# Performance work log

Hardware: AMD Instinct MI355X
Metric: run time of the kernel (lower is better)

Reference implementation:

```python
import jax, jax.numpy as jnp
import numpy as np

B, S, D, O, E = 8, 4096, 1024, 1024, 64

def setup_inputs() -> dict:
    key = jax.random.key(0)
    kx, kgw, kgb, kew, keb = jax.random.split(key, 5)
    x = jax.random.normal(kx, (B, S, D), dtype=jnp.float32)
    gate_w = jax.random.normal(kgw, (E, D), dtype=jnp.float32) * 0.02
    gate_b = jnp.zeros((E,), dtype=jnp.float32)
    expert_w = jax.random.normal(kew, (E, D, O), dtype=jnp.float32) * 0.02
    expert_b = jnp.zeros((E, O), dtype=jnp.float32)
    return {"x": x, "gate_w": gate_w, "gate_b": gate_b,
            "expert_w": expert_w, "expert_b": expert_b}

def reference(x, gate_w, gate_b, expert_w, expert_b):
    # x: [B,S,D] -> flatten tokens. With world_size=1 the all-reduce and
    # all-to-alls in the torch module are identities, and per-chunk processing
    # is token-independent, so one global pass is mathematically identical.
    b, s, d = x.shape
    xt = x.reshape(-1, d)                                   # [N, D]
    logits = xt @ gate_w.T + gate_b                         # [N, E]
    gates = jax.nn.softmax(logits, axis=-1)
    sel = jnp.argmax(gates, axis=-1)                        # [N] top-1 expert
    order = jnp.argsort(sel)                                # stable sort by expert
    xs = xt[order]                                          # tokens grouped by expert
    counts = jnp.bincount(sel, length=E).astype(jnp.int32)  # tokens per expert
    # Grouped expert GEMM: row block e of xs multiplies expert_w[e].
    ys = jax.lax.ragged_dot(xs, expert_w, counts)           # [N, O]
    ys = ys + expert_b[sel[order]]
    # Combine: scatter sorted outputs back to original token positions.
    # (Note: torch output is NOT scaled by gate probability.)
    out = jnp.zeros((xt.shape[0], expert_w.shape[-1]), dtype=ys.dtype)
    out = out.at[order].set(ys)
    return out.reshape(b, s, -1)
```

## Files before the change

### kernel.cpp

```cpp
#include <hip/hip_runtime.h>
#include <hip/hip_bf16.h>

#define N_TOK 32768
#define DIM 1024
#define OUTD 1024
#define NEXP 64

typedef __attribute__((ext_vector_type(4))) float f32x4;
typedef __attribute__((ext_vector_type(8))) short bf16x8;

__device__ __forceinline__ unsigned short f2bf(float f) {
    unsigned int u = __builtin_bit_cast(unsigned int, f);
    u += 0x7FFFu + ((u >> 16) & 1u);
    return (unsigned short)(u >> 16);
}

#define GLOAD16(gp, lp) \
    __builtin_amdgcn_global_load_lds((const __attribute__((address_space(1))) void*)(gp), \
                                     (__attribute__((address_space(3))) void*)(lp), 16, 0, 0)

__global__ __launch_bounds__(256) void prep_kernel(const float* __restrict__ x,
        const float* __restrict__ gw, const float* __restrict__ gb,
        const float* __restrict__ ew,
        int* __restrict__ sel, int* __restrict__ nflag, int* __restrict__ flags,
        int* __restrict__ counts,
        unsigned short* __restrict__ xb, unsigned short* __restrict__ wt)
{
    __shared__ __align__(16) char smem[18688];
    int tid = threadIdx.x;

    if (blockIdx.x < 512) {
        float (*xs)[36]  = (float(*)[36])smem;
        float (*wsm)[36] = (float(*)[36])(smem + 9216);
        int* h = (int*)(smem + 18432);
        if (tid < NEXP) h[tid] = 0;
        int t0 = blockIdx.x * 64;
        int tg = tid >> 4, eg = tid & 15;

        float acc[4][4];
#pragma unroll
        for (int i = 0; i < 4; i++)
#pragma unroll
            for (int j = 0; j < 4; j++) acc[i][j] = 0.f;

        for (int k0 = 0; k0 < DIM; k0 += 32) {
            __syncthreads();
#pragma unroll
            for (int q = 0; q < 2; q++) {
                int cidx = tid + q * 256;
                int r = cidx >> 3, c4 = (cidx & 7) * 4;
                *reinterpret_cast<float4*>(&xs[r][c4]) =
                    *reinterpret_cast<const float4*>(&x[(size_t)(t0 + r) * DIM + k0 + c4]);
                *reinterpret_cast<float4*>(&wsm[r][c4]) =
                    *reinterpret_cast<const float4*>(&gw[(size_t)r * DIM + k0 + c4]);
            }
            __syncthreads();
            if (xb) {
                int r = tid >> 2, cc = (tid & 3) * 8;
                float4 v0 = *reinterpret_cast<const float4*>(&xs[r][cc]);
                float4 v1 = *reinterpret_cast<const float4*>(&xs[r][cc + 4]);
                uint4 p;
                p.x = (unsigned int)f2bf(v0.x) | ((unsigned int)f2bf(v0.y) << 16);
                p.y = (unsigned int)f2bf(v0.z) | ((unsigned int)f2bf(v0.w) << 16);
                p.z = (unsigned int)f2bf(v1.x) | ((unsigned int)f2bf(v1.y) << 16);
                p.w = (unsigned int)f2bf(v1.z) | ((unsigned int)f2bf(v1.w) << 16);
                *reinterpret_cast<uint4*>(&xb[(size_t)(t0 + r) * DIM + k0 + cc]) = p;
            }
#pragma unroll
            for (int kk4 = 0; kk4 < 8; kk4++) {
                float4 xv[4], wv[4];
#pragma unroll
                for (int i = 0; i < 4; i++)
                    xv[i] = *reinterpret_cast<const float4*>(&xs[tg + 16 * i][kk4 * 4]);
#pragma unroll
                for (int j = 0; j < 4; j++)
                    wv[j] = *reinterpret_cast<const float4*>(&wsm[eg + 16 * j][kk4 * 4]);
#pragma unroll
                for (int i = 0; i < 4; i++)
#pragma unroll
                    for (int j = 0; j < 4; j++) {
                        acc[i][j] = fmaf(xv[i].x, wv[j].x, acc[i][j]);
                        acc[i][j] = fmaf(xv[i].y, wv[j].y, acc[i][j]);
                        acc[i][j] = fmaf(xv[i].z, wv[j].z, acc[i][j]);
                        acc[i][j] = fmaf(xv[i].w, wv[j].w, acc[i][j]);
                    }
            }
        }
#pragma unroll
        for (int j = 0; j < 4; j++) {
            float b = gb[eg + 16 * j];
#pragma unroll
            for (int i = 0; i < 4; i++) acc[i][j] += b;
        }
#pragma unroll
        for (int i = 0; i < 4; i++) {
            float m1 = -1e30f, m2 = -1e30f; int e1 = 0;
#pragma unroll
            for (int j = 0; j < 4; j++) {
                float v = acc[i][j]; int e = eg + 16 * j;
                if (v > m1) { m2 = m1; m1 = v; e1 = e; }
                else if (v > m2) m2 = v;
            }
#pragma unroll
            for (int d = 1; d < 16; d <<= 1) {
                float om1 = __shfl_xor(m1, d, 16);
                float om2 = __shfl_xor(m2, d, 16);
                int   oe1 = __shfl_xor(e1, d, 16);
                if (om1 > m1 || (om1 == m1 && oe1 < e1)) {
                    m2 = fmaxf(om2, m1); m1 = om1; e1 = oe1;
                } else {
                    m2 = fmaxf(m2, om1);
                }
            }
            if (eg == 0) {
                int t = t0 + tg + 16 * i;
                sel[t] = e1;
                atomicAdd(&h[e1], 1);
                if (m1 - m2 < 1e-3f) {
                    int idx = atomicAdd(nflag, 1);
                    if (idx < 4096) flags[idx] = t;
                }
            }
        }
        __syncthreads();
        if (tid < NEXP && h[tid]) atomicAdd(&counts[tid], h[tid]);
    } else {
        if (!wt) return;
        unsigned short* ts = (unsigned short*)smem;
        int lin = blockIdx.x - 512;
        int e = lin >> 8;
        int d0 = (lin & 15) * 64, o0 = ((lin >> 4) & 15) * 64;
        const float* src = ew + (size_t)e * (DIM * OUTD);
        int og = tid & 7;
        int dl = tid >> 3;
#pragma unroll
        for (int i = 0; i < 2; i++) {
            int d = dl + 32 * i;
            const float* sr = &src[(size_t)(d0 + d) * OUTD + o0 + og * 8];
            float4 v0 = *reinterpret_cast<const float4*>(sr);
            float4 v1 = *reinterpret_cast<const float4*>(sr + 4);
            unsigned short b[8] = { f2bf(v0.x), f2bf(v0.y), f2bf(v0.z), f2bf(v0.w),
                                    f2bf(v1.x), f2bf(v1.y), f2bf(v1.z), f2bf(v1.w) };
            int dg = d >> 3, dr = d & 7;
#pragma unroll
            for (int k = 0; k < 8; k++) {
                int o = og * 8 + k;
                int key = (o & 7) ^ ((o >> 3) & 7);
                ts[o * 72 + ((dg ^ key) << 3) + dr] = b[k];
            }
        }
        __syncthreads();
        unsigned short* dst = wt + (size_t)e * (DIM * OUTD);
        int dc = tid & 7;
        int ol = tid >> 3;
#pragma unroll
        for (int i = 0; i < 2; i++) {
            int o = ol + 32 * i;
            int key = (o & 7) ^ ((o >> 3) & 7);
            uint4 v = *reinterpret_cast<const uint4*>(&ts[o * 72 + ((dc ^ key) << 3)]);
            *reinterpret_cast<uint4*>(&dst[(size_t)(o0 + o) * DIM + d0 + dc * 8]) = v;
        }
    }
}

__global__ __launch_bounds__(64) void gate_fix_kernel(const float* __restrict__ x,
        const float* __restrict__ gw, const float* __restrict__ gb,
        int* __restrict__ sel, const int* __restrict__ nflag, const int* __restrict__ flags,
        int* __restrict__ counts)
{
    int n = *nflag; if (n > 4096) n = 4096;
    int b = blockIdx.x;
    if (b >= n) return;
    int t = flags[b];
    int e = threadIdx.x;
    const float* xr = x + (size_t)t * DIM;
    const float* wr = gw + (size_t)e * DIM;
    double acc = (double)gb[e];
    for (int k = 0; k < DIM; k += 4) {
        acc += (double)xr[k]   * (double)wr[k];
        acc += (double)xr[k+1] * (double)wr[k+1];
        acc += (double)xr[k+2] * (double)wr[k+2];
        acc += (double)xr[k+3] * (double)wr[k+3];
    }
    double m1 = acc; int e1 = e;
#pragma unroll
    for (int d = 1; d < 64; d <<= 1) {
        double om1 = __shfl_xor(m1, d, 64);
        int   oe1  = __shfl_xor(e1, d, 64);
        if (om1 > m1 || (om1 == m1 && oe1 < e1)) { m1 = om1; e1 = oe1; }
    }
    if (e == 0) {
        int eOld = sel[t];
        if (eOld != e1) {
            sel[t] = e1;
            atomicSub(&counts[eOld], 1);
            atomicAdd(&counts[e1], 1);
        }
    }
}

__global__ void sched_kernel(const int* __restrict__ counts, int* __restrict__ offsets,
                             int* __restrict__ schedE, int* __restrict__ schedR,
                             int* __restrict__ totalRB, int rowsShift)
{
    int e = threadIdx.x;
    int c = counts[e];
    int v = c;
#pragma unroll
    for (int d = 1; d < 64; d <<= 1) { int y = __shfl_up(v, d, 64); if (e >= d) v += y; }
    offsets[e] = v - c;
    if (e == 63) offsets[NEXP] = v;
    int rows = 1 << rowsShift;
    int nb = (c + rows - 1) >> rowsShift;
    int rbv = nb;
#pragma unroll
    for (int d = 1; d < 64; d <<= 1) { int y = __shfl_up(rbv, d, 64); if (e >= d) rbv += y; }
    int rbBase = rbv - nb;
    for (int i = 0; i < nb; i++) { schedE[rbBase + i] = e; schedR[rbBase + i] = i << rowsShift; }
    if (e == 63) *totalRB = rbv;
}

__global__ __launch_bounds__(256) void scatter_kernel(const int* __restrict__ sel,
        const int* __restrict__ offsets, int* __restrict__ cursor, int* __restrict__ perm)
{
    int t = blockIdx.x * 256 + threadIdx.x;
    int e = sel[t];
    int pos = offsets[e] + atomicAdd(&cursor[e], 1);
    perm[pos] = t;
}

__global__ __launch_bounds__(512) void moe_gemm3(
        const unsigned short* __restrict__ xb, const unsigned short* __restrict__ wt,
        const float* __restrict__ eb,
        const int* __restrict__ perm, const int* __restrict__ offsets,
        const int* __restrict__ counts, const int* __restrict__ schedE,
        const int* __restrict__ schedR, const int* __restrict__ totalRB,
        float* __restrict__ out)
{
    int xcd = blockIdx.x & 7;
    int slot = blockIdx.x >> 3;
    int rb = slot * 2 + (xcd >> 2);
    int cb = xcd & 3;
    if (rb >= *totalRB) return;
    int e = schedE[rb], r0 = schedR[rb];
    int cnt = counts[e], base = offsets[e];

    __shared__ __align__(16) unsigned short As[16384];
    __shared__ __align__(16) unsigned short Bs[16384];
    __shared__ int toks[256];

    int tid = threadIdx.x;
    if (tid < 256) {
        int r = r0 + tid;
        toks[tid] = (r < cnt) ? perm[base + r] : -1;
    }
    __syncthreads();

    int lane = tid & 63;
    int wv = tid >> 6;
    int wr = wv >> 2, wc = wv & 3;
    int lr = lane & 15, lg = lane >> 4;

    int rowS = tid >> 2;
    int koff = ((tid & 3) ^ ((tid >> 3) & 3)) * 8;
    int tokA1 = toks[rowS];       if (tokA1 < 0) tokA1 = 0;
    int tokA2 = toks[128 + rowS]; if (tokA2 < 0) tokA2 = 0;

    const unsigned short* wte = wt + ((size_t)e << 20);
    const unsigned short* aSrc1 = xb + (size_t)tokA1 * DIM + koff;
    const unsigned short* aSrc2 = xb + (size_t)tokA2 * DIM + koff;
    const unsigned short* bSrc1 = wte + (size_t)(cb * 256 + rowS) * DIM + koff;
    const unsigned short* bSrc2 = wte + (size_t)(cb * 256 + 128 + rowS) * DIM + koff;

    unsigned short* AsQ0 = As + wv * 512;
    unsigned short* AsQ1 = As + 4096 + wv * 512;
    unsigned short* BsQ0 = Bs + wv * 512;
    unsigned short* BsQ1 = Bs + 4096 + wv * 512;

    f32x4 acc[8][4];
#pragma unroll
    for (int m = 0; m < 8; m++)
#pragma unroll
        for (int n = 0; n < 4; n++)
#pragma unroll
            for (int c = 0; c < 4; c++) acc[m][n][c] = 0.f;

    const char* Asc = (const char*)As;
    const char* Bsc = (const char*)Bs;
    int fko = (lg ^ ((lr >> 1) & 3)) * 16;

    auto stage = [&](int buf, int k0) {
        int off = buf * 8192;
        GLOAD16(bSrc1 + k0, BsQ0 + off);
        GLOAD16(bSrc2 + k0, BsQ1 + off);
        GLOAD16(aSrc1 + k0, AsQ0 + off);
        GLOAD16(aSrc2 + k0, AsQ1 + off);
    };
    auto compute = [&](int buf) {
        int boff = buf * 16384;
        bf16x8 bfr[4];
#pragma unroll
        for (int n = 0; n < 4; n++) {
            int row = wc * 64 + n * 16 + lr;
            bfr[n] = *reinterpret_cast<const bf16x8*>(Bsc + boff + (row << 6) + fko);
        }
#pragma unroll
        for (int m = 0; m < 8; m++) {
            int row = wr * 128 + m * 16 + lr;
            bf16x8 afr = *reinterpret_cast<const bf16x8*>(Asc + boff + (row << 6) + fko);
#pragma unroll
            for (int n = 0; n < 4; n++)
                acc[m][n] = __builtin_amdgcn_mfma_f32_16x16x32_bf16(afr, bfr[n], acc[m][n], 0, 0, 0);
        }
    };

    stage(0, 0);
    stage(1, 32);

#pragma unroll 1
    for (int t = 0; t < 30; ++t) {
        asm volatile("s_waitcnt vmcnt(4)" ::: "memory");
        __builtin_amdgcn_s_barrier();
        compute(t & 1);
        __builtin_amdgcn_s_barrier();
        stage(t & 1, (t + 2) * 32);
    }
    asm volatile("s_waitcnt vmcnt(4)" ::: "memory");
    __builtin_amdgcn_s_barrier();
    compute(0);
    asm volatile("s_waitcnt vmcnt(0)" ::: "memory");
    __builtin_amdgcn_s_barrier();
    compute(1);

#pragma unroll
    for (int n = 0; n < 4; n++) {
        int oc = cb * 256 + wc * 64 + n * 16 + lr;
        float bias = eb[e * OUTD + oc];
#pragma unroll
        for (int m = 0; m < 8; m++) {
#pragma unroll
            for (int i2 = 0; i2 < 4; i2++) {
                int rr = wr * 128 + m * 16 + lg * 4 + i2;
                int tk = toks[rr];
                if (tk >= 0)
                    out[(size_t)tk * OUTD + oc] = acc[m][n][i2] + bias;
            }
        }
    }
}

__global__ __launch_bounds__(256) void moe_gemm_legacy(const float* __restrict__ x,
        const float* __restrict__ ew, const float* __restrict__ eb,
        const int* __restrict__ perm, const int* __restrict__ offsets,
        const int* __restrict__ counts, const int* __restrict__ schedE,
        const int* __restrict__ schedR, const int* __restrict__ totalRB,
        float* __restrict__ out)
{
    int rb = blockIdx.x;
    if (rb >= *totalRB) return;
    int cb = blockIdx.y;
    int e = schedE[rb], r0 = schedR[rb];
    int cnt = counts[e], base = offsets[e];

    __shared__ __align__(16) unsigned short As[128][40];
    __shared__ __align__(16) unsigned short Bs[128][40];
    __shared__ int toks[128];

    int tid = threadIdx.x;
    if (tid < 128) {
        int r = r0 + tid;
        toks[tid] = (r < cnt) ? perm[base + r] : -1;
    }
    __syncthreads();

    int lane = tid & 63;
    int wave = tid >> 6;
    int wr = wave >> 1, wc = wave & 1;
    int lr = lane & 15, lg = lane >> 4;

    f32x4 acc[4][4];
#pragma unroll
    for (int m = 0; m < 4; m++)
#pragma unroll
        for (int n = 0; n < 4; n++)
#pragma unroll
            for (int c = 0; c < 4; c++) acc[m][n][c] = 0.f;

    int aRow[4]; int aTok[4];
#pragma unroll
    for (int q = 0; q < 4; q++) {
        aRow[q] = (tid >> 3) + q * 32;
        int tk = toks[aRow[q]];
        aTok[q] = (tk < 0) ? 0 : tk;
    }
    int ac4 = tid & 7;
    int d0 = (tid >> 5) * 4;
    int o_lane = tid & 31;
    const float* wb = ew + (size_t)e * (DIM * OUTD) + (size_t)cb * 128;

    for (int k0 = 0; k0 < DIM; k0 += 32) {
        float4 av[4];
#pragma unroll
        for (int q = 0; q < 4; q++)
            av[q] = *reinterpret_cast<const float4*>(&x[(size_t)aTok[q] * DIM + k0 + ac4 * 4]);
        float bv[4][4];
#pragma unroll
        for (int i2 = 0; i2 < 4; i2++)
#pragma unroll
            for (int j = 0; j < 4; j++)
                bv[i2][j] = wb[(size_t)(k0 + d0 + i2) * OUTD + o_lane + 32 * j];

        __syncthreads();
#pragma unroll
        for (int q = 0; q < 4; q++) {
            uint2 p;
            p.x = (unsigned int)f2bf(av[q].x) | ((unsigned int)f2bf(av[q].y) << 16);
            p.y = (unsigned int)f2bf(av[q].z) | ((unsigned int)f2bf(av[q].w) << 16);
            *reinterpret_cast<uint2*>(&As[aRow[q]][ac4 * 4]) = p;
        }
#pragma unroll
        for (int j = 0; j < 4; j++) {
            uint2 p;
            p.x = (unsigned int)f2bf(bv[0][j]) | ((unsigned int)f2bf(bv[1][j]) << 16);
            p.y = (unsigned int)f2bf(bv[2][j]) | ((unsigned int)f2bf(bv[3][j]) << 16);
            *reinterpret_cast<uint2*>(&Bs[o_lane + 32 * j][d0]) = p;
        }
        __syncthreads();

        bf16x8 bfr[4];
#pragma unroll
        for (int n = 0; n < 4; n++)
            bfr[n] = *reinterpret_cast<const bf16x8*>(&Bs[wc * 64 + n * 16 + lr][lg * 8]);
#pragma unroll
        for (int m = 0; m < 4; m++) {
            bf16x8 afr = *reinterpret_cast<const bf16x8*>(&As[wr * 64 + m * 16 + lr][lg * 8]);
#pragma unroll
            for (int n = 0; n < 4; n++)
                acc[m][n] = __builtin_amdgcn_mfma_f32_16x16x32_bf16(afr, bfr[n], acc[m][n], 0, 0, 0);
        }
    }

#pragma unroll
    for (int n = 0; n < 4; n++) {
        int oc = cb * 128 + wc * 64 + n * 16 + lr;
        float bias = eb[e * OUTD + oc];
#pragma unroll
        for (int m = 0; m < 4; m++) {
#pragma unroll
            for (int i2 = 0; i2 < 4; i2++) {
                int rr = wr * 64 + m * 16 + lg * 4 + i2;
                int tk = toks[rr];
                if (tk >= 0)
                    out[(size_t)tk * OUTD + oc] = acc[m][n][i2] + bias;
            }
        }
    }
}

extern "C" void kernel_launch(void* const* d_in, const int* in_sizes, int n_in,
                              void* d_out, int out_size, void* d_ws, size_t ws_size,
                              hipStream_t stream)
{
    const float* x  = (const float*)d_in[0];
    const float* gw = (const float*)d_in[1];
    const float* gb = (const float*)d_in[2];
    const float* ew = (const float*)d_in[3];
    const float* eb = (const float*)d_in[4];
    float* out = (float*)d_out;

    char* ws = (char*)d_ws;
    int* counts  = (int*)(ws + 0);
    int* cursor  = (int*)(ws + 256);
    int* offsets = (int*)(ws + 512);
    int* totalRB = (int*)(ws + 1024);
    int* nflag   = (int*)(ws + 1028);
    int* flags   = (int*)(ws + 1032);
    int* schedE  = (int*)(ws + 20480);
    int* schedR  = (int*)(ws + 22528);
    int* sel     = (int*)(ws + 24576);
    int* perm    = (int*)(ws + 155648);

    const size_t WT_OFF   = (size_t)1 << 20;
    const size_t WT_BYTES = (size_t)NEXP * DIM * OUTD * 2;
    const size_t XB_OFF   = WT_OFF + WT_BYTES;
    const size_t XB_BYTES = (size_t)N_TOK * DIM * 2;
    int mode = (ws_size >= XB_OFF + XB_BYTES) ? 2 : 0;
    unsigned short* wt = (mode == 2) ? (unsigned short*)(ws + WT_OFF) : nullptr;
    unsigned short* xb = (mode == 2) ? (unsigned short*)(ws + XB_OFF) : nullptr;

    hipMemsetAsync(ws, 0, 2048, stream);

    prep_kernel<<<dim3(512 + ((mode == 2) ? 16384 : 0)), 256, 0, stream>>>(
        x, gw, gb, ew, sel, nflag, flags, counts, xb, wt);
    gate_fix_kernel<<<dim3(4096), 64, 0, stream>>>(x, gw, gb, sel, nflag, flags, counts);
    sched_kernel<<<dim3(1), 64, 0, stream>>>(counts, offsets, schedE, schedR, totalRB,
                                             (mode == 2) ? 8 : 7);
    scatter_kernel<<<dim3(N_TOK / 256), 256, 0, stream>>>(sel, offsets, cursor, perm);

    if (mode == 2)
        moe_gemm3<<<dim3(768), 512, 0, stream>>>(xb, wt, eb, perm, offsets, counts,
                                                 schedE, schedR, totalRB, out);
    else
        moe_gemm_legacy<<<dim3(320, 8), 256, 0, stream>>>(x, ew, eb, perm, offsets, counts,
                                                          schedE, schedR, totalRB, out);
}
```

Measured before the change: 438.6 us.

## Remap MoE GEMM blocks to XCDs, drop token LDS table, add MFMA priority

```diff
diff --git a/kernel.cpp b/kernel.cpp
--- a/kernel.cpp
+++ b/kernel.cpp
@@ -229,7 +229,7 @@
     perm[pos] = t;
 }
 
-__global__ __launch_bounds__(512) void moe_gemm3(
+__global__ __launch_bounds__(512, 4) void moe_gemm5(
         const unsigned short* __restrict__ xb, const unsigned short* __restrict__ wt,
         const float* __restrict__ eb,
         const int* __restrict__ perm, const int* __restrict__ offsets,
@@ -237,25 +237,19 @@
         const int* __restrict__ schedR, const int* __restrict__ totalRB,
         float* __restrict__ out)
 {
-    int xcd = blockIdx.x & 7;
-    int slot = blockIdx.x >> 3;
-    int rb = slot * 2 + (xcd >> 2);
-    int cb = xcd & 3;
+    int idx = blockIdx.x;
+    int xcd = idx & 7;
+    int s = idx >> 3;
+    int cb = s & 3;
+    int rb = (s >> 2) * 8 + xcd;
     if (rb >= *totalRB) return;
     int e = schedE[rb], r0 = schedR[rb];
     int cnt = counts[e], base = offsets[e];
 
     __shared__ __align__(16) unsigned short As[16384];
     __shared__ __align__(16) unsigned short Bs[16384];
-    __shared__ int toks[256];
 
     int tid = threadIdx.x;
-    if (tid < 256) {
-        int r = r0 + tid;
-        toks[tid] = (r < cnt) ? perm[base + r] : -1;
-    }
-    __syncthreads();
-
     int lane = tid & 63;
     int wv = tid >> 6;
     int wr = wv >> 2, wc = wv & 3;
@@ -263,8 +257,9 @@
 
     int rowS = tid >> 2;
     int koff = ((tid & 3) ^ ((tid >> 3) & 3)) * 8;
-    int tokA1 = toks[rowS];       if (tokA1 < 0) tokA1 = 0;
-    int tokA2 = toks[128 + rowS]; if (tokA2 < 0) tokA2 = 0;
+    int rA1 = r0 + rowS, rA2 = r0 + 128 + rowS;
+    int tokA1 = (rA1 < cnt) ? perm[base + rA1] : 0;
+    int tokA2 = (rA2 < cnt) ? perm[base + rA2] : 0;
 
     const unsigned short* wte = wt + ((size_t)e << 20);
     const unsigned short* aSrc1 = xb + (size_t)tokA1 * DIM + koff;
@@ -304,6 +299,7 @@
             int row = wc * 64 + n * 16 + lr;
             bfr[n] = *reinterpret_cast<const bf16x8*>(Bsc + boff + (row << 6) + fko);
         }
+        __builtin_amdgcn_s_setprio(1);
 #pragma unroll
         for (int m = 0; m < 8; m++) {
             int row = wr * 128 + m * 16 + lr;
@@ -312,6 +308,7 @@
             for (int n = 0; n < 4; n++)
                 acc[m][n] = __builtin_amdgcn_mfma_f32_16x16x32_bf16(afr, bfr[n], acc[m][n], 0, 0, 0);
         }
+        __builtin_amdgcn_s_setprio(0);
     };
 
     stage(0, 0);
@@ -332,18 +329,23 @@
     __builtin_amdgcn_s_barrier();
     compute(1);
 
-#pragma unroll
-    for (int n = 0; n < 4; n++) {
-        int oc = cb * 256 + wc * 64 + n * 16 + lr;
-        float bias = eb[e * OUTD + oc];
-#pragma unroll
-        for (int m = 0; m < 8; m++) {
-#pragma unroll
-            for (int i2 = 0; i2 < 4; i2++) {
-                int rr = wr * 128 + m * 16 + lg * 4 + i2;
-                int tk = toks[rr];
-                if (tk >= 0)
-                    out[(size_t)tk * OUTD + oc] = acc[m][n][i2] + bias;
+    float bias[4];
+#pragma unroll
+    for (int n = 0; n < 4; n++)
+        bias[n] = eb[e * OUTD + cb * 256 + wc * 64 + n * 16 + lr];
+#pragma unroll
+    for (int m = 0; m < 8; m++) {
+        int rowLoc = wr * 128 + m * 16 + lg * 4;
+#pragma unroll
+        for (int i2 = 0; i2 < 4; i2++) {
+            int r = r0 + rowLoc + i2;
+            if (r < cnt) {
+                int tk = perm[base + r];
+#pragma unroll
+                for (int n = 0; n < 4; n++) {
+                    int oc = cb * 256 + wc * 64 + n * 16 + lr;
+                    out[(size_t)tk * OUTD + oc] = acc[m][n][i2] + bias[n];
+                }
             }
         }
     }
@@ -498,7 +500,7 @@
     scatter_kernel<<<dim3(N_TOK / 256), 256, 0, stream>>>(sel, offsets, cursor, perm);
 
     if (mode == 2)
-        moe_gemm3<<<dim3(768), 512, 0, stream>>>(xb, wt, eb, perm, offsets, counts,
+        moe_gemm5<<<dim3(768), 512, 0, stream>>>(xb, wt, eb, perm, offsets, counts,
                                                  schedE, schedR, totalRB, out);
     else
         moe_gemm_legacy<<<dim3(320, 8), 256, 0, stream>>>(x, ew, eb, perm, offsets, counts,
```

Measured after the change: 1.077 ms. +145.4%, slower.
